# Performance work log

Measured on AMD Instinct MI355X. Metric: run time of the kernel, lower is better.

## Reference

```python
import jax, jax.numpy as jnp
import numpy as np

B, S, D, H = 16, 512, 1024, 4096
TOP_K = H // 4  # default: hidden_dim // 4


def setup_inputs() -> dict:
    key = jax.random.key(0)
    ks = jax.random.split(key, 11)
    s = lambda fan_in: 1.0 / np.sqrt(fan_in)
    return {
        "inputs": jax.random.normal(ks[0], (B, S, D), jnp.float32),
        "up_w": jax.random.uniform(ks[1], (H, D), jnp.float32, -s(D), s(D)),
        "up_b": jax.random.uniform(ks[2], (H,), jnp.float32, -s(D), s(D)),
        "gate_w1": jax.random.uniform(ks[3], (H, D), jnp.float32, -s(D), s(D)),
        "gate_b1": jax.random.uniform(ks[4], (H,), jnp.float32, -s(D), s(D)),
        "gate_w2": jax.random.uniform(ks[5], (H, H), jnp.float32, -s(H), s(H)),
        "gate_b2": jax.random.uniform(ks[6], (H,), jnp.float32, -s(H), s(H)),
        "mod_w": jax.random.uniform(ks[7], (H, D), jnp.float32, -s(D), s(D)),
        "mod_b": jax.random.uniform(ks[8], (H,), jnp.float32, -s(D), s(D)),
        "down_w": jax.random.uniform(ks[9], (D, H), jnp.float32, -s(H), s(H)),
        "down_b": jax.random.uniform(ks[10], (D,), jnp.float32, -s(H), s(H)),
    }


def reference(inputs, up_w, up_b, gate_w1, gate_b1, gate_w2, gate_b2,
              mod_w, mod_b, down_w, down_b):
    b, s_len, d = inputs.shape
    h_dim = up_w.shape[0]
    # gate MLP -> scores [B, S, H]
    scores = jax.nn.relu(jnp.einsum('bsd,hd->bsh', inputs, gate_w1) + gate_b1)
    scores = jnp.einsum('bsh,gh->bsg', scores, gate_w2) + gate_b2
    flat = scores.reshape(b, s_len * h_dim)
    k = min(TOP_K * s_len, s_len * h_dim)
    _, flat_idx = jax.lax.top_k(flat, k)                    # [B, k]
    hidden_idx = flat_idx % h_dim                           # [B, k]
    # mask[b, h] = True if row h of up.weight was overwritten by mod.weight
    # (duplicate indices write the same value, so set-semantics are exact)
    mask = jnp.zeros((b, h_dim), bool).at[
        jnp.arange(b)[:, None], hidden_idx].set(True)       # [B, H]
    # Instead of materializing per-batch [B,H,D] weights, compute both shared-
    # weight GEMMs and select per (batch, hidden) row — identical math.
    h_up = jnp.einsum('bsd,hd->bsh', inputs, up_w) + up_b
    h_mod = jnp.einsum('bsd,hd->bsh', inputs, mod_w) + mod_b
    h = jnp.where(mask[:, None, :], h_mod, h_up)            # [B, S, H]
    h = jax.nn.silu(h)
    # dropout is identity in eval/reference mode
    return jnp.einsum('bsh,dh->bsd', h, down_w) + down_b
```

## Files before the change

### kernel.cpp

```cpp
#include <hip/hip_runtime.h>
#include <cstdint>

typedef __attribute__((ext_vector_type(4))) _Float16 f16x4;
typedef __attribute__((ext_vector_type(8))) _Float16 f16x8;
typedef __attribute__((ext_vector_type(4))) float f32x4;

#define D_DIM 1024
#define H_DIM 4096
#define BS_ROWS 8192
#define K_SEL 524288u
#define CAND_CAP 32768u

__device__ __forceinline__ unsigned lkey(float v){
  float u = fmaf(v, 67108864.f, 268435456.f);
  u = fminf(fmaxf(u, 0.f), 536870911.f);
  return (unsigned)u;
}

__device__ __forceinline__ void gload16(const _Float16* g, _Float16* l){
  __builtin_amdgcn_global_load_lds(
      (const __attribute__((address_space(1))) void*)g,
      (__attribute__((address_space(3))) void*)l, 16, 0, 0);
}

template<int N> __device__ __forceinline__ void waitcnt_vm(){
  if      constexpr (N == 0) asm volatile("s_waitcnt vmcnt(0)" ::: "memory");
  else if constexpr (N == 4) asm volatile("s_waitcnt vmcnt(4)" ::: "memory");
  else if constexpr (N == 6) asm volatile("s_waitcnt vmcnt(6)" ::: "memory");
  else                       asm volatile("s_waitcnt vmcnt(8)" ::: "memory");
}

__device__ __forceinline__ size_t img_g32(int row, int k8, int nkt32){
  int p = (row & 127) >> 1;
  int s = (((row & 1) << 2) | (k8 & 3)) ^ (p & 7);
  return ((size_t)((row >> 7) * nkt32 + (k8 >> 2)) << 9) + (p << 3) + s;
}

__global__ __launch_bounds__(256)
void pack_all(const float* __restrict__ X, const float* __restrict__ g1w,
              const float* __restrict__ g2w, const float* __restrict__ upw,
              const float* __restrict__ modw, const float* __restrict__ dww,
              _Float16* __restrict__ Xhi, _Float16* __restrict__ Xlo,
              _Float16* __restrict__ G1hi, _Float16* __restrict__ G1lo,
              _Float16* __restrict__ G2hi, _Float16* __restrict__ G2lo,
              _Float16* __restrict__ UPhi, _Float16* __restrict__ MODhi,
              _Float16* __restrict__ DWhi)
{
  unsigned g = blockIdx.x * 256u + threadIdx.x;
  const float* W; _Float16* hi; _Float16* lo = nullptr;
  int k8s, n32; unsigned base;
  if      (g < 1048576u){ W=X;    hi=Xhi;  lo=Xlo;  k8s=7; n32=32;  base=0u;        }
  else if (g < 1572864u){ W=g1w;  hi=G1hi; lo=G1lo; k8s=7; n32=32;  base=1048576u; }
  else if (g < 3670016u){ W=g2w;  hi=G2hi; lo=G2lo; k8s=9; n32=128; base=1572864u; }
  else if (g < 4194304u){ W=upw;  hi=UPhi;          k8s=7; n32=32;  base=3670016u; }
  else if (g < 4718592u){ W=modw; hi=MODhi;         k8s=7; n32=32;  base=4194304u; }
  else                  { W=dww;  hi=DWhi;          k8s=9; n32=128; base=4718592u; }
  g -= base;
  int row = (int)(g >> k8s), k8 = (int)(g & ((1u << k8s) - 1u));
  const float* src = W + ((size_t)row << (k8s + 3)) + (k8 << 3);
  float4 f0 = *(const float4*)src, f1 = *(const float4*)(src + 4);
  float ff[8] = {f0.x,f0.y,f0.z,f0.w,f1.x,f1.y,f1.z,f1.w};
  f16x8 hv, lv;
  #pragma unroll
  for (int i = 0; i < 8; i++){
    hv[i] = (_Float16)ff[i];
    lv[i] = (_Float16)(ff[i] - (float)hv[i]);
  }
  size_t d = img_g32(row, k8, n32) << 3;
  *(f16x8*)&hi[d] = hv;
  if (lo) *(f16x8*)&lo[d] = lv;
}

enum { MODE_G1 = 0, MODE_G2 = 1, MODE_UPMOD = 2, MODE_DOWN = 3 };

template<int MODE>
__global__ __launch_bounds__(256)
void gemm_t(const _Float16* __restrict__ Ahi, const _Float16* __restrict__ Alo,
            const _Float16* __restrict__ Bhi, const _Float16* __restrict__ Blo,
            const float* __restrict__ bias0, const float* __restrict__ bias1,
            const unsigned* __restrict__ mask,
            _Float16* __restrict__ Chi, _Float16* __restrict__ Clo,
            float* __restrict__ C32,
            unsigned* __restrict__ keys, unsigned* __restrict__ Mkey,
            unsigned* __restrict__ hist,
            int N, int K, int m_img_base, int c_row_base, int batch_base)
{
  constexpr int NSEG = (MODE == MODE_G1) ? 3 : 1;
  constexpr bool BSEL = (MODE == MODE_UPMOD);
  constexpr int NLD = (NSEG == 3) ? 8 : 4;
  constexpr int DEPTH = (NSEG == 3) ? 2 : 3;
  __shared__ __align__(16) _Float16 sA [DEPTH][4096];
  __shared__ __align__(16) _Float16 sB [DEPTH][4096];
  __shared__ __align__(16) _Float16 sAl[NSEG == 3 ? 2 : 1][NSEG == 3 ? 4096 : 8];
  __shared__ __align__(16) _Float16 sBl[NSEG == 3 ? 2 : 1][NSEG == 3 ? 4096 : 8];

  const int nbx = gridDim.x;
  const int h = blockIdx.y * nbx + blockIdx.x;
  const int xcd = h & 7, idx = h >> 3;
  const int cw = nbx >> 2;
  const int ch = gridDim.y >> 1;
  const int bx = (xcd & 3) * cw + idx % cw;
  const int by = (xcd >> 2) * ch + idx / cw;

  const int tid = threadIdx.x;
  const int lane = tid & 63;
  const int w  = tid >> 6;
  const int wr = w >> 1, wc = w & 1;
  const int lr = lane & 15;
  const int q  = lane >> 4;

  const int m0 = m_img_base + by * 128;
  const int n0 = bx * 128;
  const int nkt = K >> 5;
  const size_t arow = (size_t)(m0 >> 7) * nkt;
  const size_t brow = (size_t)(n0 >> 7) * nkt;

  const _Float16* bsrcl[2];
  if (BSEL){
    const int bb = m0 >> 9;
    #pragma unroll
    for (int j = 0; j < 2; j++){
      int gi = (w*2 + j)*64 + lane;
      int p = gi >> 3, x = (gi & 7) ^ (p & 7);
      int row = (p << 1) | (x >> 2);
      bsrcl[j] = (mask[bb * H_DIM + n0 + row] ? Blo : Bhi) + (gi << 3);
    }
    waitcnt_vm<0>();
  }

  f32x4 acc[4][4];
  #pragma unroll
  for (int i = 0; i < 4; i++)
    #pragma unroll
    for (int j = 0; j < 4; j++) acc[i][j] = (f32x4){0.f,0.f,0.f,0.f};

  const int soff = (((((lr & 1) << 2) | q) ^ (lr >> 1)) << 3);

  auto STAGE = [&](int buf, int kt){
    const _Float16* at = Ahi + ((arow + kt) << 12);
    #pragma unroll
    for (int j = 0; j < 2; j++)
      gload16(at + ((w*2 + j) << 9) + (lane << 3), &sA[buf][(w*2 + j) << 9]);
    if (NSEG == 3){
      const _Float16* alt = Alo + ((arow + kt) << 12);
      const _Float16* bht = Bhi + ((brow + kt) << 12);
      const _Float16* blt = Blo + ((brow + kt) << 12);
      #pragma unroll
      for (int j = 0; j < 2; j++){
        gload16(alt + ((w*2 + j) << 9) + (lane << 3), &sAl[buf][(w*2 + j) << 9]);
        gload16(bht + ((w*2 + j) << 9) + (lane << 3), &sB [buf][(w*2 + j) << 9]);
        gload16(blt + ((w*2 + j) << 9) + (lane << 3), &sBl[buf][(w*2 + j) << 9]);
      }
    } else if (BSEL){
      const size_t toff = (brow + kt) << 12;
      #pragma unroll
      for (int j = 0; j < 2; j++)
        gload16(bsrcl[j] + toff, &sB[buf][(w*2 + j) << 9]);
    } else {
      const _Float16* bht = Bhi + ((brow + kt) << 12);
      #pragma unroll
      for (int j = 0; j < 2; j++)
        gload16(bht + ((w*2 + j) << 9) + (lane << 3), &sB[buf][(w*2 + j) << 9]);
    }
  };

  STAGE(0, 0);
  if (DEPTH == 3) STAGE(1, 1);

  for (int kt = 0; kt < nkt; ++kt){
    const int rem = nkt - 1 - kt;
    const int cur = (DEPTH == 2) ? (kt & 1) : (kt % 3);
    if (DEPTH == 2){
      if (rem >= 1){ STAGE((kt + 1) & 1, kt + 1); waitcnt_vm<NLD>(); }
      else         { waitcnt_vm<0>(); }
    } else {
      if (rem >= 2){ STAGE((kt + 2) % 3, kt + 2); waitcnt_vm<8>(); }
      else if (rem == 1){ waitcnt_vm<4>(); }
      else         { waitcnt_vm<0>(); }
    }
    __builtin_amdgcn_s_barrier();
    __builtin_amdgcn_sched_barrier(0);

    f16x8 fah[4], fbh[4], fal[4], fbl[4];
    #pragma unroll
    for (int i = 0; i < 4; i++){
      const int ap = ((wr*32 + i*8 + (lr >> 1)) << 6) + soff;
      const int bp = ((wc*32 + i*8 + (lr >> 1)) << 6) + soff;
      fah[i] = *(const f16x8*)&sA[cur][ap];
      fbh[i] = *(const f16x8*)&sB[cur][bp];
      if (NSEG == 3){
        fal[i] = *(const f16x8*)&sAl[cur][ap];
        fbl[i] = *(const f16x8*)&sBl[cur][bp];
      }
    }
    #pragma unroll
    for (int mi = 0; mi < 4; mi++)
      #pragma unroll
      for (int ni = 0; ni < 4; ni++)
        acc[mi][ni] = __builtin_amdgcn_mfma_f32_16x16x32_f16(fah[mi], fbh[ni], acc[mi][ni], 0,0,0);
    if (NSEG == 3){
      #pragma unroll
      for (int mi = 0; mi < 4; mi++)
        #pragma unroll
        for (int ni = 0; ni < 4; ni++)
          acc[mi][ni] = __builtin_amdgcn_mfma_f32_16x16x32_f16(fal[mi], fbh[ni], acc[mi][ni], 0,0,0);
      #pragma unroll
      for (int mi = 0; mi < 4; mi++)
        #pragma unroll
        for (int ni = 0; ni < 4; ni++)
          acc[mi][ni] = __builtin_amdgcn_mfma_f32_16x16x32_f16(fah[mi], fbl[ni], acc[mi][ni], 0,0,0);
    }
    __builtin_amdgcn_s_barrier();
  }

  unsigned* lh = (unsigned*)&sA[0][0];
  if (MODE == MODE_G2){
    __syncthreads();
    for (int i = tid; i < 4096; i += 256) lh[i] = 0;
    __syncthreads();
  }

  #pragma unroll
  for (int ni = 0; ni < 4; ni++){
    const int gc = n0 + wc*64 + ni*16 + lr;
    float bias;
    if (MODE == MODE_UPMOD) bias = mask[(m0 >> 9) * H_DIM + gc] ? bias1[gc] : bias0[gc];
    else                    bias = bias0[gc];
    unsigned colmax = 0u;
    #pragma unroll
    for (int mi = 0; mi < 4; mi++){
      #pragma unroll
      for (int r = 0; r < 4; r++){
        const int gr = m0 + wr*64 + mi*16 + q*4 + r;
        const int cr = gr - c_row_base;
        float v = acc[mi][ni][r] + bias;
        if (MODE == MODE_G1){
          v = fmaxf(v, 0.f);
          size_t d = (img_g32(cr, gc >> 3, N >> 5) << 3) + (gc & 7);
          Chi[d] = (_Float16)v;
        }
        if (MODE == MODE_UPMOD){
          v = v / (1.f + __expf(-v));
          size_t d = (img_g32(cr, gc >> 3, N >> 5) << 3) + (gc & 7);
          Chi[d] = (_Float16)v;
        }
        if (MODE == MODE_DOWN) C32[(size_t)cr * N + gc] = v;
        if (MODE == MODE_G2){
          unsigned key = lkey(v);
          keys[(size_t)cr * N + gc] = key;
          colmax = max(colmax, key);
          atomicAdd(&lh[key >> 17], 1u);
        }
      }
    }
    if (MODE == MODE_G2)
      atomicMax(&Mkey[(batch_base + (m0 >> 9)) * H_DIM + gc], colmax);
  }

  if (MODE == MODE_G2){
    __syncthreads();
    const int gb = batch_base + (m0 >> 9);
    for (int i = tid; i < 4096; i += 256)
      if (lh[i]) atomicAdd(&hist[(gb << 12) + i], lh[i]);
  }
}


__global__ __launch_bounds__(256)
void select12(const unsigned* __restrict__ hist, unsigned* __restrict__ b12,
              unsigned* __restrict__ krem, unsigned* __restrict__ ccount, int b0)
{
  const int b = b0 + (int)blockIdx.x;
  __shared__ unsigned part[256];
  const unsigned base = (unsigned)b << 12;
  unsigned s = 0;
  #pragma unroll
  for (int i = 0; i < 16; i++) s += hist[base + threadIdx.x*16 + i];
  part[threadIdx.x] = s;
  __syncthreads();
  if (threadIdx.x == 0){
    unsigned cum = 0; int t = 255;
    for (; t > 0; --t){
      if (cum + part[t] >= K_SEL) break;
      cum += part[t];
    }
    int bin = 15; unsigned kr = K_SEL;
    for (; bin > 0; --bin){
      unsigned c = hist[base + t*16 + bin];
      if (cum + c >= K_SEL) break;
      cum += c;
    }
    kr = K_SEL - cum;
    b12[b] = (unsigned)(t*16 + bin);
    krem[b] = kr;
    ccount[b] = 0;
  }
}

__global__ __launch_bounds__(256)
void collect(const unsigned* __restrict__ keys, const unsigned* __restrict__ b12,
             unsigned* __restrict__ cand, unsigned* __restrict__ ccount, int b0)
{
  __shared__ unsigned cbuf[1024];
  __shared__ unsigned lcnt, gbase;
  const int bl = blockIdx.y;
  const int b  = b0 + bl;
  const unsigned bin = b12[b];
  if (threadIdx.x == 0) lcnt = 0;
  __syncthreads();
  const uint4* p = (const uint4*)(keys + (size_t)bl*2097152u + (size_t)blockIdx.x*8192u);
  uint4 kv[8];
  #pragma unroll
  for (int j = 0; j < 8; j++) kv[j] = p[threadIdx.x + j*256];
  #pragma unroll
  for (int j = 0; j < 8; j++){
    #pragma unroll
    for (int e = 0; e < 4; e++){
      unsigned k = (e==0)?kv[j].x:(e==1)?kv[j].y:(e==2)?kv[j].z:kv[j].w;
      if ((k >> 17) == bin){
        unsigned idx = atomicAdd(&lcnt, 1u);
        if (idx < 1024u) cbuf[idx] = k;
      }
    }
  }
  __syncthreads();
  const unsigned n = lcnt < 1024u ? lcnt : 1024u;
  if (threadIdx.x == 0) gbase = atomicAdd(&ccount[b], n);
  __syncthreads();
  const unsigned gb = gbase;
  for (unsigned i = threadIdx.x; i < n; i += 256){
    unsigned dst = gb + i;
    if (dst < CAND_CAP) cand[((size_t)b << 15) + dst] = cbuf[i];
  }
}

__global__ __launch_bounds__(256)
void select_exact(const unsigned* __restrict__ cand, const unsigned* __restrict__ ccount,
                  const unsigned* __restrict__ b12, const unsigned* __restrict__ kremA,
                  unsigned* __restrict__ tkey, int b0)
{
  const int b = b0 + (int)blockIdx.x;
  unsigned cc = ccount[b];
  const unsigned n = cc < CAND_CAP ? cc : CAND_CAP;
  __shared__ unsigned h[256];
  __shared__ unsigned sh2[2];
  unsigned prefix = b12[b] << 17;
  unsigned krem = kremA[b];
  const unsigned pm[3]  = {0xFFFE0000u, 0xFFFFFE00u, 0xFFFFFFFEu};
  const int      shs[3] = {9, 1, 0};
  const int      wid[3] = {256, 256, 2};
  for (int pass = 0; pass < 3; ++pass){
    if (threadIdx.x < (unsigned)wid[pass]) h[threadIdx.x] = 0;
    __syncthreads();
    for (unsigned i = threadIdx.x; i < n; i += 256){
      unsigned k = cand[((size_t)b << 15) + i];
      if ((k & pm[pass]) == prefix)
        atomicAdd(&h[(k >> shs[pass]) & (unsigned)(wid[pass]-1)], 1u);
    }
    __syncthreads();
    if (threadIdx.x == 0){
      unsigned cum = 0; int bin = wid[pass]-1;
      for (; bin > 0; --bin){
        unsigned c = h[bin];
        if (cum + c >= krem) break;
        cum += c;
      }
      krem -= cum;
      prefix |= ((unsigned)bin) << shs[pass];
      sh2[0] = prefix; sh2[1] = krem;
    }
    __syncthreads();
    prefix = sh2[0]; krem = sh2[1];
    __syncthreads();
  }
  if (threadIdx.x == 0) tkey[b] = prefix;
}

__global__ __launch_bounds__(256)
void make_mask(const unsigned* __restrict__ Mkey, const unsigned* __restrict__ tkey,
               unsigned* __restrict__ mask){
  const int i = blockIdx.x * 256 + threadIdx.x;
  const int b = i >> 12;
  mask[i] = (Mkey[i] >= tkey[b]) ? 1u : 0u;
}

extern "C" void kernel_launch(void* const* d_in, const int* in_sizes, int n_in,
                              void* d_out, int out_size, void* d_ws, size_t ws_size,
                              hipStream_t stream)
{
  (void)in_sizes; (void)n_in; (void)out_size; (void)ws_size;
  const float* X      = (const float*)d_in[0];
  const float* up_w   = (const float*)d_in[1];
  const float* up_b   = (const float*)d_in[2];
  const float* g1w    = (const float*)d_in[3];
  const float* g1b    = (const float*)d_in[4];
  const float* g2w    = (const float*)d_in[5];
  const float* g2b    = (const float*)d_in[6];
  const float* mod_w  = (const float*)d_in[7];
  const float* mod_b  = (const float*)d_in[8];
  const float* down_w = (const float*)d_in[9];
  const float* down_b = (const float*)d_in[10];
  float* out = (float*)d_out;

  char* ws = (char*)d_ws;
  _Float16* Xhi  = (_Float16*)(ws);
  _Float16* Xlo  = (_Float16*)(ws + (16ull<<20));
  _Float16* G1hi = (_Float16*)(ws + (32ull<<20));
  _Float16* G1lo = (_Float16*)(ws + (40ull<<20));
  _Float16* G2hi = (_Float16*)(ws + (48ull<<20));
  _Float16* UPhi = (_Float16*)(ws + (112ull<<20));
  _Float16* MODhi= (_Float16*)(ws + (120ull<<20));
  _Float16* DWhi = (_Float16*)(ws + (128ull<<20));
  _Float16* Fhi  = (_Float16*)(ws + (136ull<<20));
  unsigned* keys = (unsigned*)(ws + (168ull<<20));
  _Float16* Hbuf = (_Float16*)(ws + (136ull<<20));
  char* aux = ws + (232ull<<20);
  unsigned* Mkey  = (unsigned*)(aux);
  unsigned* maskb = (unsigned*)(aux + 262144);
  unsigned* hist  = (unsigned*)(aux + 524288);
  unsigned* cand  = (unsigned*)(aux + 786432);
  unsigned* b12   = (unsigned*)(aux + 786432 + 2097152);
  unsigned* krem  = (unsigned*)(aux + 786432 + 2097152 + 64);
  unsigned* ccnt  = (unsigned*)(aux + 786432 + 2097152 + 128);
  unsigned* tkey  = (unsigned*)(aux + 786432 + 2097152 + 192);

  pack_all<<<20480, 256, 0, stream>>>(X, g1w, g2w, up_w, mod_w, down_w,
                                      Xhi, Xlo, G1hi, G1lo, G2hi, nullptr,
                                      UPhi, MODhi, DWhi);

  hipMemsetAsync(Mkey, 0, 262144, stream);
  hipMemsetAsync(hist, 0, 262144, stream);

  for (int half = 0; half < 2; ++half){
    const int b0 = half * 8;
    gemm_t<MODE_G1><<<dim3(32, 32), 256, 0, stream>>>(
        Xhi, Xlo, G1hi, G1lo, g1b, nullptr, nullptr,
        Fhi, nullptr, nullptr, nullptr, nullptr, nullptr,
        H_DIM, D_DIM, half*4096, half*4096, 0);
    gemm_t<MODE_G2><<<dim3(32, 32), 256, 0, stream>>>(
        Fhi, nullptr, G2hi, nullptr, g2b, nullptr, nullptr,
        nullptr, nullptr, nullptr, keys, Mkey, hist,
        H_DIM, H_DIM, 0, 0, b0);
    select12<<<8, 256, 0, stream>>>(hist, b12, krem, ccnt, b0);
    collect<<<dim3(256, 8), 256, 0, stream>>>(keys, b12, cand, ccnt, b0);
    select_exact<<<8, 256, 0, stream>>>(cand, ccnt, b12, krem, tkey, b0);
  }
  make_mask<<<256, 256, 0, stream>>>(Mkey, tkey, maskb);

  gemm_t<MODE_UPMOD><<<dim3(32, 64), 256, 0, stream>>>(
      Xhi, nullptr, UPhi, MODhi, up_b, mod_b, maskb,
      Hbuf, nullptr, nullptr, nullptr, nullptr, nullptr,
      H_DIM, D_DIM, 0, 0, 0);
  gemm_t<MODE_DOWN><<<dim3(8, 64), 256, 0, stream>>>(
      Hbuf, nullptr, DWhi, nullptr, down_b, nullptr, nullptr,
      nullptr, nullptr, out, nullptr, nullptr, nullptr,
      D_DIM, H_DIM, 0, 0, 0);
}
```

Baseline: 963.5 us.

## Add dedicated 256x256-tile 512-thread kernel for the gate-2 GEMM

Moves the largest GEMM (gate layer 2, K=4096) out of the generic 128x128 templated kernel into its own kernel. The new kernel uses 256x256 tiles, 8 waves, and a 3-stage LDS pipeline whose loads are interleaved into four MFMA phases with barriers and setprio. The goal is more operand reuse per loaded byte and better overlap of global-to-LDS loads with compute. The fused epilogue (key encoding, column max, histogram) is carried over unchanged. The trade-off is a grid of only 256 blocks per half and heavier LDS and register use.

```diff
diff --git a/kernel.cpp b/kernel.cpp
--- a/kernel.cpp
+++ b/kernel.cpp
@@ -81,9 +81,7 @@
             const unsigned* __restrict__ mask,
             _Float16* __restrict__ Chi, _Float16* __restrict__ Clo,
             float* __restrict__ C32,
-            unsigned* __restrict__ keys, unsigned* __restrict__ Mkey,
-            unsigned* __restrict__ hist,
-            int N, int K, int m_img_base, int c_row_base, int batch_base)
+            int N, int K, int m_img_base, int c_row_base)
 {
   constexpr int NSEG = (MODE == MODE_G1) ? 3 : 1;
   constexpr bool BSEL = (MODE == MODE_UPMOD);
@@ -213,20 +211,12 @@
     __builtin_amdgcn_s_barrier();
   }
 
-  unsigned* lh = (unsigned*)&sA[0][0];
-  if (MODE == MODE_G2){
-    __syncthreads();
-    for (int i = tid; i < 4096; i += 256) lh[i] = 0;
-    __syncthreads();
-  }
-
   #pragma unroll
   for (int ni = 0; ni < 4; ni++){
     const int gc = n0 + wc*64 + ni*16 + lr;
     float bias;
     if (MODE == MODE_UPMOD) bias = mask[(m0 >> 9) * H_DIM + gc] ? bias1[gc] : bias0[gc];
     else                    bias = bias0[gc];
-    unsigned colmax = 0u;
     #pragma unroll
     for (int mi = 0; mi < 4; mi++){
       #pragma unroll
@@ -245,24 +235,132 @@
           Chi[d] = (_Float16)v;
         }
         if (MODE == MODE_DOWN) C32[(size_t)cr * N + gc] = v;
-        if (MODE == MODE_G2){
-          unsigned key = lkey(v);
-          keys[(size_t)cr * N + gc] = key;
-          colmax = max(colmax, key);
-          atomicAdd(&lh[key >> 17], 1u);
-        }
       }
     }
-    if (MODE == MODE_G2)
-      atomicMax(&Mkey[(batch_base + (m0 >> 9)) * H_DIM + gc], colmax);
-  }
-
-  if (MODE == MODE_G2){
-    __syncthreads();
-    const int gb = batch_base + (m0 >> 9);
-    for (int i = tid; i < 4096; i += 256)
-      if (lh[i]) atomicAdd(&hist[(gb << 12) + i], lh[i]);
-  }
+  }
+}
+
+__global__ __launch_bounds__(512, 2)
+void gemm_g2(const _Float16* __restrict__ A, const _Float16* __restrict__ B,
+             const float* __restrict__ bias0,
+             unsigned* __restrict__ keys, unsigned* __restrict__ Mkey,
+             unsigned* __restrict__ hist, int N, int K, int batch_base)
+{
+  __shared__ __align__(16) _Float16 sAb[3][8192];
+  __shared__ __align__(16) _Float16 sBb[3][8192];
+
+  const int nbx = gridDim.x;
+  const int h = blockIdx.y * nbx + blockIdx.x;
+  const int xcd = h & 7, idx = h >> 3;
+  const int cw = nbx >> 2, ch = gridDim.y >> 1;
+  const int bx = (xcd & 3) * cw + idx % cw;
+  const int by = (xcd >> 2) * ch + idx / cw;
+
+  const int tid = threadIdx.x;
+  const int lane = tid & 63;
+  const int w = tid >> 6;
+  const int wrow = w >> 2, wcol = w & 3;
+  const int lr = lane & 15;
+  const int q = lane >> 4;
+
+  const int m0 = by * 256;
+  const int n0 = bx * 256;
+  const int nkt = K >> 5;
+  const int ar0 = (m0 >> 7) * nkt;
+  const int br0 = (n0 >> 7) * nkt;
+
+  f32x4 acc[8][4];
+  #pragma unroll
+  for (int i = 0; i < 8; i++)
+    #pragma unroll
+    for (int j = 0; j < 4; j++) acc[i][j] = (f32x4){0.f,0.f,0.f,0.f};
+
+  const int soff = (((((lr & 1) << 2) | q) ^ (lr >> 1)) << 3);
+  int offA[8], offB[4];
+  #pragma unroll
+  for (int mi = 0; mi < 8; mi++) offA[mi] = ((mi*8 + (lr >> 1)) << 6) + soff;
+  #pragma unroll
+  for (int ni = 0; ni < 4; ni++)
+    offB[ni] = (((wcol & 1)*32 + ni*8 + (lr >> 1)) << 6) + soff;
+  const int arb = wrow * 4096;
+  const int bcb = (wcol >> 1) * 4096;
+
+  auto STA = [&](int buf, int rb, int kt){
+    gload16(A + ((((size_t)(ar0 + rb*nkt + kt) << 9) + tid) << 3),
+            &sAb[buf][rb*4096 + (tid << 3)]);
+  };
+  auto STB = [&](int buf, int cb, int kt){
+    gload16(B + ((((size_t)(br0 + cb*nkt + kt) << 9) + tid) << 3),
+            &sBb[buf][cb*4096 + (tid << 3)]);
+  };
+
+#define G2PHASE(P, STG)                                                        \
+  {                                                                            \
+    f16x8 a0 = *(const f16x8*)&sAb[cur][arb + offA[2*(P)]];                    \
+    f16x8 a1 = *(const f16x8*)&sAb[cur][arb + offA[2*(P)+1]];                  \
+    STG;                                                                       \
+    if ((P) == 3){ if (pf) waitcnt_vm<4>(); else waitcnt_vm<0>(); }            \
+    __builtin_amdgcn_s_barrier();                                              \
+    asm volatile("s_waitcnt lgkmcnt(0)" ::: "memory");                         \
+    __builtin_amdgcn_sched_barrier(0);                                         \
+    __builtin_amdgcn_s_setprio(1);                                             \
+    _Pragma("unroll")                                                          \
+    for (int ni = 0; ni < 4; ni++)                                             \
+      acc[2*(P)][ni]   = __builtin_amdgcn_mfma_f32_16x16x32_f16(a0, fb[ni], acc[2*(P)][ni], 0,0,0);   \
+    _Pragma("unroll")                                                          \
+    for (int ni = 0; ni < 4; ni++)                                             \
+      acc[2*(P)+1][ni] = __builtin_amdgcn_mfma_f32_16x16x32_f16(a1, fb[ni], acc[2*(P)+1][ni], 0,0,0); \
+    __builtin_amdgcn_s_setprio(0);                                             \
+    __builtin_amdgcn_s_barrier();                                              \
+  }
+
+  STA(0,0,0); STB(0,0,0); STB(0,1,0); STA(0,1,0);
+  STA(1,0,1); STB(1,0,1); STB(1,1,1); STA(1,1,1);
+  waitcnt_vm<4>();
+  __builtin_amdgcn_s_barrier();
+
+  for (int kt = 0; kt < nkt; ++kt){
+    const int cur = kt % 3, nb = (kt + 2) % 3;
+    const bool pf = (kt + 2 < nkt);
+    f16x8 fb[4];
+    #pragma unroll
+    for (int ni = 0; ni < 4; ni++)
+      fb[ni] = *(const f16x8*)&sBb[cur][bcb + offB[ni]];
+    G2PHASE(0, if (pf) STA(nb, 0, kt+2))
+    G2PHASE(1, if (pf) STB(nb, 0, kt+2))
+    G2PHASE(2, if (pf) STB(nb, 1, kt+2))
+    G2PHASE(3, if (pf) STA(nb, 1, kt+2))
+  }
+#undef G2PHASE
+
+  unsigned* lh = (unsigned*)&sAb[0][0];
+  __syncthreads();
+  for (int i = tid; i < 4096; i += 512) lh[i] = 0;
+  __syncthreads();
+
+  const int gb = batch_base + (m0 >> 9);
+  #pragma unroll
+  for (int ni = 0; ni < 4; ni++){
+    const int gc = n0 + wcol*64 + ni*16 + lr;
+    const float bias = bias0[gc];
+    unsigned colmax = 0u;
+    #pragma unroll
+    for (int mi = 0; mi < 8; mi++){
+      #pragma unroll
+      for (int r = 0; r < 4; r++){
+        const int gr = m0 + wrow*128 + mi*16 + q*4 + r;
+        float v = acc[mi][ni][r] + bias;
+        unsigned key = lkey(v);
+        keys[(size_t)gr * N + gc] = key;
+        colmax = max(colmax, key);
+        atomicAdd(&lh[key >> 17], 1u);
+      }
+    }
+    atomicMax(&Mkey[gb * H_DIM + gc], colmax);
+  }
+  __syncthreads();
+  for (int i = tid; i < 4096; i += 512)
+    if (lh[i]) atomicAdd(&hist[(gb << 12) + i], lh[i]);
 }
 
 
@@ -435,12 +533,9 @@
     const int b0 = half * 8;
     gemm_t<MODE_G1><<<dim3(32, 32), 256, 0, stream>>>(
         Xhi, Xlo, G1hi, G1lo, g1b, nullptr, nullptr,
-        Fhi, nullptr, nullptr, nullptr, nullptr, nullptr,
-        H_DIM, D_DIM, half*4096, half*4096, 0);
-    gemm_t<MODE_G2><<<dim3(32, 32), 256, 0, stream>>>(
-        Fhi, nullptr, G2hi, nullptr, g2b, nullptr, nullptr,
-        nullptr, nullptr, nullptr, keys, Mkey, hist,
-        H_DIM, H_DIM, 0, 0, b0);
+        Fhi, nullptr, nullptr, H_DIM, D_DIM, half*4096, half*4096);
+    gemm_g2<<<dim3(16, 16), 512, 0, stream>>>(
+        Fhi, G2hi, g2b, keys, Mkey, hist, H_DIM, H_DIM, b0);
     select12<<<8, 256, 0, stream>>>(hist, b12, krem, ccnt, b0);
     collect<<<dim3(256, 8), 256, 0, stream>>>(keys, b12, cand, ccnt, b0);
     select_exact<<<8, 256, 0, stream>>>(cand, ccnt, b12, krem, tkey, b0);
@@ -449,10 +544,8 @@
 
   gemm_t<MODE_UPMOD><<<dim3(32, 64), 256, 0, stream>>>(
       Xhi, nullptr, UPhi, MODhi, up_b, mod_b, maskb,
-      Hbuf, nullptr, nullptr, nullptr, nullptr, nullptr,
-      H_DIM, D_DIM, 0, 0, 0);
+      Hbuf, nullptr, nullptr, H_DIM, D_DIM, 0, 0);
   gemm_t<MODE_DOWN><<<dim3(8, 64), 256, 0, stream>>>(
       Hbuf, nullptr, DWhi, nullptr, down_b, nullptr, nullptr,
-      nullptr, nullptr, out, nullptr, nullptr, nullptr,
-      D_DIM, H_DIM, 0, 0, 0);
-}
+      nullptr, nullptr, out, D_DIM, H_DIM, 0, 0);
+}
```

Result: faster. 912.0 us, median of 2 (-5.3%).
